# Optimization experiments

Hardware: AMD Instinct MI355X
Metric: run time of the kernel (lower is better)

## Reference

```python
import jax, jax.numpy as jnp
import numpy as np

N, E = 50000, 800000
HID, EDIM, HEADS = 256, 64, 8
C = HID // HEADS  # per-head channels = 32
NEG_SLOPE = 0.2
LN_EPS = 1e-5


def setup_inputs() -> dict:
    key = jax.random.key(0)
    ks = jax.random.split(key, 12)
    s = 1.0 / np.sqrt(HID)
    se = 1.0 / np.sqrt(EDIM)
    return {
        "x": jax.random.normal(ks[0], (N, HID), jnp.float32),
        "edge_index": jax.random.randint(ks[1], (2, E), 0, N, jnp.int32),
        "edge_attr": jax.random.normal(ks[2], (E, EDIM), jnp.float32),
        "W": jax.random.uniform(ks[3], (HID, HEADS * C), jnp.float32, -s, s),
        "W_e": jax.random.uniform(ks[4], (EDIM, HEADS * C), jnp.float32, -se, se),
        "att_src": jax.random.normal(ks[5], (HEADS, C), jnp.float32) * 0.1,
        "att_dst": jax.random.normal(ks[6], (HEADS, C), jnp.float32) * 0.1,
        "att_edge": jax.random.normal(ks[7], (HEADS, C), jnp.float32) * 0.1,
        "bias": jnp.zeros((HEADS * C,), jnp.float32),
        "gamma": jnp.ones((HID,), jnp.float32),
        "beta": jnp.zeros((HID,), jnp.float32),
    }


def _gat_block(x, edge_index, edge_attr, W, W_e, att_src, att_dst, att_edge, bias, gamma, beta):
    n = x.shape[0]
    src, dst = edge_index[0], edge_index[1]
    # node projection (shared for src/dst, as in PyG GATConv non-bipartite)
    xp = (x @ W).reshape(n, HEADS, C)                       # [N,H,C]
    a_src = jnp.einsum("nhc,hc->nh", xp, att_src)          # [N,H]
    a_dst = jnp.einsum("nhc,hc->nh", xp, att_dst)          # [N,H]
    ep = (edge_attr @ W_e).reshape(-1, HEADS, C)            # [E,H,C]
    a_edge = jnp.einsum("ehc,hc->eh", ep, att_edge)        # [E,H]
    # per-edge attention logit + LeakyReLU
    alpha = a_src[src] + a_dst[dst] + a_edge                # [E,H]
    alpha = jax.nn.leaky_relu(alpha, NEG_SLOPE)
    # segment softmax over incoming edges of each dst node
    m = jax.ops.segment_max(alpha, dst, num_segments=n)     # [N,H]
    m = jnp.where(jnp.isfinite(m), m, 0.0)
    ea = jnp.exp(alpha - m[dst])
    den = jax.ops.segment_sum(ea, dst, num_segments=n)      # [N,H]
    attn = ea / (den[dst] + 1e-16)                          # [E,H]
    # weighted message + scatter-add
    msg = xp[src] * attn[:, :, None]                        # [E,H,C]
    out = jax.ops.segment_sum(msg, dst, num_segments=n)     # [N,H,C]
    h = out.reshape(n, HEADS * C) + bias
    # residual + LayerNorm (dropout in eval mode -> identity)
    y = x + h
    mu = jnp.mean(y, axis=-1, keepdims=True)
    var = jnp.var(y, axis=-1, keepdims=True)
    return (y - mu) * jax.lax.rsqrt(var + LN_EPS) * gamma + beta


def reference(x, edge_index, edge_attr, W, W_e, att_src, att_dst, att_edge, bias, gamma, beta):
    return _gat_block(x, edge_index, edge_attr, W, W_e, att_src, att_dst, att_edge, bias, gamma, beta)
```

## Files before the change

kernel.cpp:

```cpp
#include <hip/hip_runtime.h>
#include <cstdint>

#define NEG_SLOPE 0.2f
#define LN_EPS 1e-5f

typedef __bf16 bf16x8 __attribute__((ext_vector_type(8)));
typedef float f32x4 __attribute__((ext_vector_type(4)));

__device__ __forceinline__ float b2f(unsigned int u) {
    union { unsigned int i; float f; } x; x.i = u << 16; return x.f;
}
__device__ __forceinline__ unsigned short f2b(float f) {
    union { float f; unsigned int i; } x; x.f = f;
    unsigned int r = x.i + 0x7fffu + ((x.i >> 16) & 1u);
    return (unsigned short)(r >> 16);
}

__global__ void k0a_prep(const float* __restrict__ W,
                         const float* __restrict__ We,
                         const float* __restrict__ att_src,
                         const float* __restrict__ att_dst,
                         const float* __restrict__ att_edge,
                         float* __restrict__ u_src, float* __restrict__ u_dst,
                         float* __restrict__ vW) {
    int t = threadIdx.x;
    const float* wr = W + t * 256;
    for (int h = 0; h < 8; h++) {
        float s1 = 0.f, s2 = 0.f;
        for (int c = 0; c < 32; c++) {
            float w = wr[h * 32 + c];
            s1 += w * att_src[h * 32 + c];
            s2 += w * att_dst[h * 32 + c];
        }
        u_src[t * 8 + h] = s1; u_dst[t * 8 + h] = s2;
    }
    if (t < 64) {
        const float* er = We + t * 256;
        for (int h = 0; h < 8; h++) {
            float s = 0.f;
            for (int c = 0; c < 32; c++) s += er[h * 32 + c] * att_edge[h * 32 + c];
            vW[t * 8 + h] = s;
        }
    }
}

__global__ void k0b_wfrag(const float* __restrict__ W,
                          unsigned short* __restrict__ Wf) {
    int T = blockIdx.x * 256 + threadIdx.x;
    int j    = T & 7;
    int lane = (T >> 3) & 63;
    int kk   = (T >> 9) & 7;
    int i    = (T >> 12) & 3;
    int w    = T >> 14;
    int n = w * 64 + i * 16 + (lane & 15);
    int k = kk * 32 + (lane >> 4) * 8 + j;
    Wf[T] = f2b(W[k * 256 + n]);
}

__global__ __launch_bounds__(256) void k_deg(const int* __restrict__ ei,
                                             int* __restrict__ deg, int E) {
    int e = blockIdx.x * 256 + threadIdx.x;
    if (e < E) atomicAdd(deg + ei[E + e], 1);
}

__global__ __launch_bounds__(256) void k1_xp(const float* __restrict__ x,
                                             const unsigned short* __restrict__ Wf,
                                             const float* __restrict__ u_src,
                                             const float* __restrict__ u_dst,
                                             unsigned short* __restrict__ xp,
                                             float* __restrict__ a_src,
                                             float* __restrict__ a_dst, int N) {
    __shared__ float red[2][4][16][8];
    int m0 = blockIdx.x * 16;
    int lane = threadIdx.x & 63, wave = threadIdx.x >> 6;
    int quad = lane >> 4, l16 = lane & 15;
    int mrow = m0 + l16; if (mrow > N - 1) mrow = N - 1;
    const float* ap = x + (size_t)mrow * 256 + quad * 8;
    const unsigned short* wfw = Wf + (size_t)wave * 16384;
    f32x4 ac0 = {0,0,0,0}, ac1 = {0,0,0,0}, ac2 = {0,0,0,0}, ac3 = {0,0,0,0};
    float pas[8] = {0,0,0,0,0,0,0,0}, pad_[8] = {0,0,0,0,0,0,0,0};
#pragma unroll
    for (int kk = 0; kk < 8; kk++) {
        float4 fa0 = *(const float4*)(ap + kk * 32);
        float4 fa1 = *(const float4*)(ap + kk * 32 + 4);
        if ((kk >> 1) == wave) {
            float f[8] = {fa0.x, fa0.y, fa0.z, fa0.w, fa1.x, fa1.y, fa1.z, fa1.w};
#pragma unroll
            for (int j = 0; j < 8; j++) {
                int k = kk * 32 + quad * 8 + j;
                const float4* up = (const float4*)(u_src + k * 8);
                float4 s0 = up[0], s1 = up[1];
                const float4* vp = (const float4*)(u_dst + k * 8);
                float4 d0 = vp[0], d1 = vp[1];
                pas[0] += f[j] * s0.x; pas[1] += f[j] * s0.y;
                pas[2] += f[j] * s0.z; pas[3] += f[j] * s0.w;
                pas[4] += f[j] * s1.x; pas[5] += f[j] * s1.y;
                pas[6] += f[j] * s1.z; pas[7] += f[j] * s1.w;
                pad_[0] += f[j] * d0.x; pad_[1] += f[j] * d0.y;
                pad_[2] += f[j] * d0.z; pad_[3] += f[j] * d0.w;
                pad_[4] += f[j] * d1.x; pad_[5] += f[j] * d1.y;
                pad_[6] += f[j] * d1.z; pad_[7] += f[j] * d1.w;
            }
        }
        union { unsigned short u[8]; bf16x8 v; } A;
        A.u[0] = f2b(fa0.x); A.u[1] = f2b(fa0.y); A.u[2] = f2b(fa0.z); A.u[3] = f2b(fa0.w);
        A.u[4] = f2b(fa1.x); A.u[5] = f2b(fa1.y); A.u[6] = f2b(fa1.z); A.u[7] = f2b(fa1.w);
        const unsigned short* wk = wfw + kk * 512 + lane * 8;
        bf16x8 b0 = *(const bf16x8*)(wk);
        bf16x8 b1 = *(const bf16x8*)(wk + 4096);
        bf16x8 b2 = *(const bf16x8*)(wk + 8192);
        bf16x8 b3 = *(const bf16x8*)(wk + 12288);
        ac0 = __builtin_amdgcn_mfma_f32_16x16x32_bf16(A.v, b0, ac0, 0, 0, 0);
        ac1 = __builtin_amdgcn_mfma_f32_16x16x32_bf16(A.v, b1, ac1, 0, 0, 0);
        ac2 = __builtin_amdgcn_mfma_f32_16x16x32_bf16(A.v, b2, ac2, 0, 0, 0);
        ac3 = __builtin_amdgcn_mfma_f32_16x16x32_bf16(A.v, b3, ac3, 0, 0, 0);
    }
#pragma unroll
    for (int h = 0; h < 8; h++) {
        pas[h] += __shfl_xor(pas[h], 16, 64);
        pas[h] += __shfl_xor(pas[h], 32, 64);
        pad_[h] += __shfl_xor(pad_[h], 16, 64);
        pad_[h] += __shfl_xor(pad_[h], 32, 64);
    }
    if (quad == 0) {
#pragma unroll
        for (int h = 0; h < 8; h++) {
            red[0][wave][l16][h] = pas[h];
            red[1][wave][l16][h] = pad_[h];
        }
    }
    int nb = wave * 64;
#pragma unroll
    for (int r = 0; r < 4; r++) {
        int m = m0 + quad * 4 + r;
        if (m < N) {
            unsigned short* op = xp + (size_t)m * 256 + nb + l16;
            op[0]  = f2b(ac0[r]); op[16] = f2b(ac1[r]);
            op[32] = f2b(ac2[r]); op[48] = f2b(ac3[r]);
        }
    }
    __syncthreads();
    {
        int t = threadIdx.x;
        int arr = t >> 7, r = (t >> 3) & 15, h = t & 7;
        int m = m0 + r;
        if (m < N) {
            float sum = red[arr][0][r][h] + red[arr][1][r][h]
                      + red[arr][2][r][h] + red[arr][3][r][h];
            (arr ? a_dst : a_src)[m * 8 + h] = sum;
        }
    }
}

__global__ __launch_bounds__(256) void k2_edge(const int* __restrict__ ei,
                                               const float* __restrict__ eattr,
                                               const float* __restrict__ vW,
                                               const float* __restrict__ a_src,
                                               const float* __restrict__ a_dst,
                                               int* __restrict__ cursor,
                                               int* __restrict__ srcs,
                                               uint4* __restrict__ eav, int E) {
    __shared__ float sv[2048];
    int t = threadIdx.x;
    if (t < 128) {
        const float4* g = (const float4*)vW;
        float4* s4 = (float4*)sv;
        int k = t >> 1, half = t & 1;
        int kl = ((k & 15) << 2) | (k >> 4);
        s4[kl * 2 + half] = g[t];
    }
    __syncthreads();
    int e = blockIdx.x * 64 + (t >> 2), kp = t & 3;
    if (e >= E) return;
    const float4* ar = (const float4*)(eattr + (size_t)e * 64 + kp * 16);
    float acc[8] = {0,0,0,0,0,0,0,0};
#pragma unroll
    for (int q = 0; q < 4; q++) {
        float4 u = ar[q];
        float f[4] = {u.x, u.y, u.z, u.w};
#pragma unroll
        for (int j = 0; j < 4; j++) {
            int kl = ((q * 4 + j) << 2) | kp;
            const float4* vp = (const float4*)(sv + kl * 8);
            float4 v0 = vp[0], v1 = vp[1];
            acc[0] += f[j] * v0.x; acc[1] += f[j] * v0.y;
            acc[2] += f[j] * v0.z; acc[3] += f[j] * v0.w;
            acc[4] += f[j] * v1.x; acc[5] += f[j] * v1.y;
            acc[6] += f[j] * v1.z; acc[7] += f[j] * v1.w;
        }
    }
#pragma unroll
    for (int h = 0; h < 8; h++) {
        acc[h] += __shfl_xor(acc[h], 1, 64);
        acc[h] += __shfl_xor(acc[h], 2, 64);
    }
    int s = ei[e], d = ei[E + e];
    float2 asv = *(const float2*)(a_src + s * 8 + kp * 2);
    float2 adv = *(const float2*)(a_dst + d * 8 + kp * 2);
    float l0 = asv.x + adv.x + acc[kp * 2];
    float l1 = asv.y + adv.y + acc[kp * 2 + 1];
    l0 = (l0 > 0.f) ? l0 : NEG_SLOPE * l0;
    l1 = (l1 > 0.f) ? l1 : NEG_SLOPE * l1;
    unsigned int pk = (unsigned)f2b(__expf(l0)) | ((unsigned)f2b(__expf(l1)) << 16);
    int l = t & 63;
    int p = 0;
    if (kp == 0) p = atomicAdd(cursor + d, 1);
    p = __shfl(p, l & 60, 64);
    ((unsigned int*)eav)[(size_t)p * 4 + kp] = pk;
    if (kp == 0) srcs[p] = s;
}

__global__ __launch_bounds__(1024) void k3a_scan(const int* __restrict__ deg,
                                                 int* __restrict__ rowptr,
                                                 int* __restrict__ bsum, int N) {
    __shared__ int s[1024];
    int t = threadIdx.x, i = blockIdx.x * 1024 + t;
    int v = (i < N) ? deg[i] : 0;
    s[t] = v; __syncthreads();
    for (int off = 1; off < 1024; off <<= 1) {
        int add = (t >= off) ? s[t - off] : 0;
        __syncthreads();
        s[t] += add;
        __syncthreads();
    }
    if (i < N) rowptr[i] = s[t] - v;
    if (t == 1023) bsum[blockIdx.x] = s[1023];
}
__global__ void k3b_scan(const int* __restrict__ bsum, int* __restrict__ boff, int nb) {
    int l = threadIdx.x;
    int v = (l < nb) ? bsum[l] : 0;
    int x = v;
#pragma unroll
    for (int off = 1; off < 64; off <<= 1) {
        int y = __shfl_up(x, off, 64);
        if (l >= off) x += y;
    }
    if (l < nb) boff[l] = x - v;
}
__global__ __launch_bounds__(1024) void k3c_add(int* __restrict__ rowptr,
                                                int* __restrict__ cursor,
                                                const int* __restrict__ boff, int N, int E) {
    int i = blockIdx.x * 1024 + threadIdx.x;
    if (i < N) {
        int r = rowptr[i] + boff[blockIdx.x];
        rowptr[i] = r; cursor[i] = r;
    }
    if (i == 0) rowptr[N] = E;
}

__global__ __launch_bounds__(256) void k4_agg(const float* __restrict__ xin,
                                              const unsigned short* __restrict__ xp,
                                              const int* __restrict__ srcs,
                                              const uint4* __restrict__ eav,
                                              const int* __restrict__ rowptr,
                                              const float* __restrict__ bias,
                                              const float* __restrict__ gamma,
                                              const float* __restrict__ beta,
                                              float* __restrict__ out, int N) {
    __shared__ int ssrc[64];
    __shared__ float sea[64 * 9];
    __shared__ float racc[4][64][4];
    __shared__ float rden[8];
    int n = blockIdx.x;
    int t = threadIdx.x, wave = t >> 6, l = t & 63;
    int start = rowptr[n], end = rowptr[n + 1];
    int hh = l >> 3;
    float a0 = 0.f, a1 = 0.f, a2 = 0.f, a3 = 0.f;
    float den[8] = {0,0,0,0,0,0,0,0};
    for (int base = start; base < end; base += 64) {
        int cnt = end - base; if (cnt > 64) cnt = 64;
        if (t < cnt) {
            ssrc[t] = srcs[base + t];
            uint4 u = eav[base + t];
            float v0 = b2f(u.x & 0xffffu), v1 = b2f(u.x >> 16);
            float v2 = b2f(u.y & 0xffffu), v3 = b2f(u.y >> 16);
            float v4 = b2f(u.z & 0xffffu), v5 = b2f(u.z >> 16);
            float v6 = b2f(u.w & 0xffffu), v7 = b2f(u.w >> 16);
            float* sp = sea + t * 9;
            sp[0] = v0; sp[1] = v1; sp[2] = v2; sp[3] = v3;
            sp[4] = v4; sp[5] = v5; sp[6] = v6; sp[7] = v7;
            den[0] += v0; den[1] += v1; den[2] += v2; den[3] += v3;
            den[4] += v4; den[5] += v5; den[6] += v6; den[7] += v7;
        }
        __syncthreads();
        int i = wave;
        for (; i + 12 < cnt; i += 16) {
            int s0 = ssrc[i], s1 = ssrc[i + 4], s2 = ssrc[i + 8], s3 = ssrc[i + 12];
            uint2 u0 = *(const uint2*)(xp + (size_t)s0 * 256 + l * 4);
            uint2 u1 = *(const uint2*)(xp + (size_t)s1 * 256 + l * 4);
            uint2 u2 = *(const uint2*)(xp + (size_t)s2 * 256 + l * 4);
            uint2 u3 = *(const uint2*)(xp + (size_t)s3 * 256 + l * 4);
            float w0 = sea[i * 9 + hh],        w1 = sea[(i + 4) * 9 + hh];
            float w2 = sea[(i + 8) * 9 + hh],  w3 = sea[(i + 12) * 9 + hh];
            a0 += b2f(u0.x & 0xffffu) * w0; a1 += b2f(u0.x >> 16) * w0;
            a2 += b2f(u0.y & 0xffffu) * w0; a3 += b2f(u0.y >> 16) * w0;
            a0 += b2f(u1.x & 0xffffu) * w1; a1 += b2f(u1.x >> 16) * w1;
            a2 += b2f(u1.y & 0xffffu) * w1; a3 += b2f(u1.y >> 16) * w1;
            a0 += b2f(u2.x & 0xffffu) * w2; a1 += b2f(u2.x >> 16) * w2;
            a2 += b2f(u2.y & 0xffffu) * w2; a3 += b2f(u2.y >> 16) * w2;
            a0 += b2f(u3.x & 0xffffu) * w3; a1 += b2f(u3.x >> 16) * w3;
            a2 += b2f(u3.y & 0xffffu) * w3; a3 += b2f(u3.y >> 16) * w3;
        }
        for (; i + 4 < cnt; i += 8) {
            int s0 = ssrc[i], s1 = ssrc[i + 4];
            uint2 u0 = *(const uint2*)(xp + (size_t)s0 * 256 + l * 4);
            uint2 u1 = *(const uint2*)(xp + (size_t)s1 * 256 + l * 4);
            float w0 = sea[i * 9 + hh], w1 = sea[(i + 4) * 9 + hh];
            a0 += b2f(u0.x & 0xffffu) * w0; a1 += b2f(u0.x >> 16) * w0;
            a2 += b2f(u0.y & 0xffffu) * w0; a3 += b2f(u0.y >> 16) * w0;
            a0 += b2f(u1.x & 0xffffu) * w1; a1 += b2f(u1.x >> 16) * w1;
            a2 += b2f(u1.y & 0xffffu) * w1; a3 += b2f(u1.y >> 16) * w1;
        }
        for (; i < cnt; i += 4) {
            int s0 = ssrc[i];
            uint2 u0 = *(const uint2*)(xp + (size_t)s0 * 256 + l * 4);
            float w0 = sea[i * 9 + hh];
            a0 += b2f(u0.x & 0xffffu) * w0; a1 += b2f(u0.x >> 16) * w0;
            a2 += b2f(u0.y & 0xffffu) * w0; a3 += b2f(u0.y >> 16) * w0;
        }
        __syncthreads();
    }
    racc[wave][l][0] = a0; racc[wave][l][1] = a1;
    racc[wave][l][2] = a2; racc[wave][l][3] = a3;
    if (wave == 0) {
#pragma unroll
        for (int off = 32; off > 0; off >>= 1) {
#pragma unroll
            for (int j = 0; j < 8; j++) den[j] += __shfl_xor(den[j], off, 64);
        }
        if (l < 8) rden[l] = den[l];
    }
    __syncthreads();
    if (wave != 0) return;
    float m0 = racc[0][l][0] + racc[1][l][0] + racc[2][l][0] + racc[3][l][0];
    float m1 = racc[0][l][1] + racc[1][l][1] + racc[2][l][1] + racc[3][l][1];
    float m2 = racc[0][l][2] + racc[1][l][2] + racc[2][l][2] + racc[3][l][2];
    float m3 = racc[0][l][3] + racc[1][l][3] + racc[2][l][3] + racc[3][l][3];
    float sinv = 1.0f / (rden[hh] + 1e-16f);
    m0 *= sinv; m1 *= sinv; m2 *= sinv; m3 *= sinv;
    float4 xv = *(const float4*)(xin + (size_t)n * 256 + l * 4);
    float4 bv = *(const float4*)(bias + l * 4);
    float y0 = xv.x + m0 + bv.x;
    float y1 = xv.y + m1 + bv.y;
    float y2 = xv.z + m2 + bv.z;
    float y3 = xv.w + m3 + bv.w;
    float s1 = y0 + y1 + y2 + y3;
    float s2 = y0 * y0 + y1 * y1 + y2 * y2 + y3 * y3;
#pragma unroll
    for (int o = 32; o > 0; o >>= 1) {
        s1 += __shfl_down(s1, o, 64);
        s2 += __shfl_down(s2, o, 64);
    }
    s1 = __shfl(s1, 0, 64); s2 = __shfl(s2, 0, 64);
    float mu = s1 * (1.f / 256.f);
    float var = s2 * (1.f / 256.f) - mu * mu;
    float rs = rsqrtf(var + LN_EPS);
    float4 gv  = *(const float4*)(gamma + l * 4);
    float4 btv = *(const float4*)(beta + l * 4);
    float4 ov;
    ov.x = (y0 - mu) * rs * gv.x + btv.x;
    ov.y = (y1 - mu) * rs * gv.y + btv.y;
    ov.z = (y2 - mu) * rs * gv.z + btv.z;
    ov.w = (y3 - mu) * rs * gv.w + btv.w;
    *(float4*)(out + (size_t)n * 256 + l * 4) = ov;
}

extern "C" void kernel_launch(void* const* d_in, const int* in_sizes, int n_in,
                              void* d_out, int out_size, void* d_ws, size_t ws_size,
                              hipStream_t stream) {
    const float* x     = (const float*)d_in[0];
    const int*   ei    = (const int*)d_in[1];
    const float* eattr = (const float*)d_in[2];
    const float* W     = (const float*)d_in[3];
    const float* We    = (const float*)d_in[4];
    const float* atts  = (const float*)d_in[5];
    const float* attd  = (const float*)d_in[6];
    const float* atte  = (const float*)d_in[7];
    const float* bias  = (const float*)d_in[8];
    const float* gamma = (const float*)d_in[9];
    const float* beta  = (const float*)d_in[10];
    float* out = (float*)d_out;
    int N = in_sizes[0] / 256;
    int E = in_sizes[1] / 2;

    char* p = (char*)d_ws;
    auto carve = [&](size_t bytes) -> void* {
        void* r = (void*)p; p += (bytes + 255) & ~(size_t)255; return r;
    };
    unsigned short* xp = (unsigned short*)carve((size_t)N * 256 * 2);
    uint4* eav         = (uint4*)carve((size_t)E * 16);
    int*   srcs        = (int*)carve((size_t)E * 4);
    float* a_src       = (float*)carve((size_t)N * 8 * 4);
    float* a_dst       = (float*)carve((size_t)N * 8 * 4);
    int*   deg         = (int*)carve((size_t)N * 4);
    int*   rowptr      = (int*)carve((size_t)(N + 1) * 4);
    int*   cursor      = (int*)carve((size_t)N * 4);
    int*   bsum        = (int*)carve(1024);
    int*   boff        = (int*)carve(1024);
    float* u_src       = (float*)carve(2048 * 4);
    float* u_dst       = (float*)carve(2048 * 4);
    float* vW          = (float*)carve(512 * 4);
    unsigned short* Wf = (unsigned short*)carve(65536 * 2);

    hipMemsetAsync(deg, 0, (size_t)N * 4, stream);

    hipLaunchKernelGGL(k0a_prep, dim3(1), dim3(256), 0, stream,
                       W, We, atts, attd, atte, u_src, u_dst, vW);
    hipLaunchKernelGGL(k0b_wfrag, dim3(256), dim3(256), 0, stream, W, Wf);
    hipLaunchKernelGGL(k_deg, dim3((E + 255) / 256), dim3(256), 0, stream, ei, deg, E);
    int nb = (N + 1023) / 1024;
    hipLaunchKernelGGL(k3a_scan, dim3(nb), dim3(1024), 0, stream, deg, rowptr, bsum, N);
    hipLaunchKernelGGL(k3b_scan, dim3(1), dim3(64), 0, stream, bsum, boff, nb);
    hipLaunchKernelGGL(k3c_add, dim3(nb), dim3(1024), 0, stream, rowptr, cursor, boff, N, E);
    hipLaunchKernelGGL(k1_xp, dim3((N + 15) / 16), dim3(256), 0, stream,
                       x, Wf, u_src, u_dst, xp, a_src, a_dst, N);
    hipLaunchKernelGGL(k2_edge, dim3((E + 63) / 64), dim3(256), 0, stream,
                       ei, eattr, vW, a_src, a_dst, cursor, srcs, eav, E);
    hipLaunchKernelGGL(k4_agg, dim3(N), dim3(256), 0, stream,
                       x, xp, srcs, eav, rowptr, bias, gamma, beta, out, N);
}
```

Before: 610.6 us.

## Merge prep kernels, widen xp GEMM tile, compute attention logits from accumulators

Combines the degree count, weight-fragment packing and edge-attention vector prep into one launch, which removes two kernel launches. The node projection kernel now handles 64 rows per block, so each loaded W fragment is reused across four row groups. It computes a_src and a_dst directly from the bf16-MFMA fp32 accumulators through shuffle reductions instead of a separate fp32 dot with precomputed u vectors. This drops the u_src/u_dst precompute and the shared-memory reduction, but the logits now come from bf16-rounded inputs, a small numerical change. Output stores switch to hardware bf16 conversion.

```diff
diff --git a/kernel.cpp b/kernel.cpp
--- a/kernel.cpp
+++ b/kernel.cpp
@@ -15,139 +15,147 @@
     unsigned int r = x.i + 0x7fffu + ((x.i >> 16) & 1u);
     return (unsigned short)(r >> 16);
 }
-
-__global__ void k0a_prep(const float* __restrict__ W,
-                         const float* __restrict__ We,
-                         const float* __restrict__ att_src,
-                         const float* __restrict__ att_dst,
-                         const float* __restrict__ att_edge,
-                         float* __restrict__ u_src, float* __restrict__ u_dst,
-                         float* __restrict__ vW) {
-    int t = threadIdx.x;
-    const float* wr = W + t * 256;
-    for (int h = 0; h < 8; h++) {
-        float s1 = 0.f, s2 = 0.f;
-        for (int c = 0; c < 32; c++) {
-            float w = wr[h * 32 + c];
-            s1 += w * att_src[h * 32 + c];
-            s2 += w * att_dst[h * 32 + c];
-        }
-        u_src[t * 8 + h] = s1; u_dst[t * 8 + h] = s2;
-    }
-    if (t < 64) {
-        const float* er = We + t * 256;
-        for (int h = 0; h < 8; h++) {
-            float s = 0.f;
-            for (int c = 0; c < 32; c++) s += er[h * 32 + c] * att_edge[h * 32 + c];
-            vW[t * 8 + h] = s;
-        }
-    }
-}
-
-__global__ void k0b_wfrag(const float* __restrict__ W,
-                          unsigned short* __restrict__ Wf) {
-    int T = blockIdx.x * 256 + threadIdx.x;
-    int j    = T & 7;
-    int lane = (T >> 3) & 63;
-    int kk   = (T >> 9) & 7;
-    int i    = (T >> 12) & 3;
-    int w    = T >> 14;
-    int n = w * 64 + i * 16 + (lane & 15);
-    int k = kk * 32 + (lane >> 4) * 8 + j;
-    Wf[T] = f2b(W[k * 256 + n]);
-}
-
-__global__ __launch_bounds__(256) void k_deg(const int* __restrict__ ei,
-                                             int* __restrict__ deg, int E) {
-    int e = blockIdx.x * 256 + threadIdx.x;
-    if (e < E) atomicAdd(deg + ei[E + e], 1);
+__device__ __forceinline__ unsigned short f2b_hw(float f) {
+    __bf16 b = (__bf16)f;
+    union { __bf16 b; unsigned short u; } x; x.b = b; return x.u;
+}
+
+__global__ __launch_bounds__(256) void k0_prep(const int* __restrict__ ei,
+                                               const float* __restrict__ W,
+                                               const float* __restrict__ We,
+                                               const float* __restrict__ att_edge,
+                                               int* __restrict__ deg,
+                                               unsigned short* __restrict__ Wf,
+                                               float* __restrict__ vW,
+                                               int E, int nDegBlocks) {
+    int b = blockIdx.x;
+    if (b < nDegBlocks) {
+        int e = b * 256 + threadIdx.x;
+        if (e < E) atomicAdd(deg + ei[E + e], 1);
+    } else if (b < nDegBlocks + 256) {
+        int T = (b - nDegBlocks) * 256 + threadIdx.x;
+        int j    = T & 7;
+        int lane = (T >> 3) & 63;
+        int kk   = (T >> 9) & 7;
+        int i    = (T >> 12) & 3;
+        int w    = T >> 14;
+        int n = w * 64 + i * 16 + (lane & 15);
+        int k = kk * 32 + (lane >> 4) * 8 + j;
+        Wf[T] = f2b(W[k * 256 + n]);
+    } else {
+        int t = threadIdx.x;
+        if (t < 64) {
+            const float* er = We + t * 256;
+            for (int h = 0; h < 8; h++) {
+                float s = 0.f;
+                for (int c = 0; c < 32; c++) s += er[h * 32 + c] * att_edge[h * 32 + c];
+                vW[t * 8 + h] = s;
+            }
+        }
+    }
 }
 
 __global__ __launch_bounds__(256) void k1_xp(const float* __restrict__ x,
                                              const unsigned short* __restrict__ Wf,
-                                             const float* __restrict__ u_src,
-                                             const float* __restrict__ u_dst,
+                                             const float* __restrict__ att_src,
+                                             const float* __restrict__ att_dst,
                                              unsigned short* __restrict__ xp,
                                              float* __restrict__ a_src,
                                              float* __restrict__ a_dst, int N) {
-    __shared__ float red[2][4][16][8];
-    int m0 = blockIdx.x * 16;
+    int m0 = blockIdx.x * 64;
     int lane = threadIdx.x & 63, wave = threadIdx.x >> 6;
     int quad = lane >> 4, l16 = lane & 15;
-    int mrow = m0 + l16; if (mrow > N - 1) mrow = N - 1;
-    const float* ap = x + (size_t)mrow * 256 + quad * 8;
     const unsigned short* wfw = Wf + (size_t)wave * 16384;
-    f32x4 ac0 = {0,0,0,0}, ac1 = {0,0,0,0}, ac2 = {0,0,0,0}, ac3 = {0,0,0,0};
-    float pas[8] = {0,0,0,0,0,0,0,0}, pad_[8] = {0,0,0,0,0,0,0,0};
+    const float* ap[4];
+#pragma unroll
+    for (int g = 0; g < 4; g++) {
+        int mrow = m0 + g * 16 + l16; if (mrow > N - 1) mrow = N - 1;
+        ap[g] = x + (size_t)mrow * 256 + quad * 8;
+    }
+    f32x4 acc[4][4];
+#pragma unroll
+    for (int g = 0; g < 4; g++)
+#pragma unroll
+        for (int i = 0; i < 4; i++) acc[g][i] = (f32x4){0, 0, 0, 0};
+
 #pragma unroll
     for (int kk = 0; kk < 8; kk++) {
-        float4 fa0 = *(const float4*)(ap + kk * 32);
-        float4 fa1 = *(const float4*)(ap + kk * 32 + 4);
-        if ((kk >> 1) == wave) {
-            float f[8] = {fa0.x, fa0.y, fa0.z, fa0.w, fa1.x, fa1.y, fa1.z, fa1.w};
-#pragma unroll
-            for (int j = 0; j < 8; j++) {
-                int k = kk * 32 + quad * 8 + j;
-                const float4* up = (const float4*)(u_src + k * 8);
-                float4 s0 = up[0], s1 = up[1];
-                const float4* vp = (const float4*)(u_dst + k * 8);
-                float4 d0 = vp[0], d1 = vp[1];
-                pas[0] += f[j] * s0.x; pas[1] += f[j] * s0.y;
-                pas[2] += f[j] * s0.z; pas[3] += f[j] * s0.w;
-                pas[4] += f[j] * s1.x; pas[5] += f[j] * s1.y;
-                pas[6] += f[j] * s1.z; pas[7] += f[j] * s1.w;
-                pad_[0] += f[j] * d0.x; pad_[1] += f[j] * d0.y;
-                pad_[2] += f[j] * d0.z; pad_[3] += f[j] * d0.w;
-                pad_[4] += f[j] * d1.x; pad_[5] += f[j] * d1.y;
-                pad_[6] += f[j] * d1.z; pad_[7] += f[j] * d1.w;
-            }
-        }
-        union { unsigned short u[8]; bf16x8 v; } A;
-        A.u[0] = f2b(fa0.x); A.u[1] = f2b(fa0.y); A.u[2] = f2b(fa0.z); A.u[3] = f2b(fa0.w);
-        A.u[4] = f2b(fa1.x); A.u[5] = f2b(fa1.y); A.u[6] = f2b(fa1.z); A.u[7] = f2b(fa1.w);
         const unsigned short* wk = wfw + kk * 512 + lane * 8;
         bf16x8 b0 = *(const bf16x8*)(wk);
         bf16x8 b1 = *(const bf16x8*)(wk + 4096);
         bf16x8 b2 = *(const bf16x8*)(wk + 8192);
         bf16x8 b3 = *(const bf16x8*)(wk + 12288);
-        ac0 = __builtin_amdgcn_mfma_f32_16x16x32_bf16(A.v, b0, ac0, 0, 0, 0);
-        ac1 = __builtin_amdgcn_mfma_f32_16x16x32_bf16(A.v, b1, ac1, 0, 0, 0);
-        ac2 = __builtin_amdgcn_mfma_f32_16x16x32_bf16(A.v, b2, ac2, 0, 0, 0);
-        ac3 = __builtin_amdgcn_mfma_f32_16x16x32_bf16(A.v, b3, ac3, 0, 0, 0);
-    }
-#pragma unroll
-    for (int h = 0; h < 8; h++) {
-        pas[h] += __shfl_xor(pas[h], 16, 64);
-        pas[h] += __shfl_xor(pas[h], 32, 64);
-        pad_[h] += __shfl_xor(pad_[h], 16, 64);
-        pad_[h] += __shfl_xor(pad_[h], 32, 64);
-    }
-    if (quad == 0) {
-#pragma unroll
-        for (int h = 0; h < 8; h++) {
-            red[0][wave][l16][h] = pas[h];
-            red[1][wave][l16][h] = pad_[h];
-        }
-    }
+#pragma unroll
+        for (int g = 0; g < 4; g++) {
+            float4 fa0 = *(const float4*)(ap[g] + kk * 32);
+            float4 fa1 = *(const float4*)(ap[g] + kk * 32 + 4);
+            bf16x8 Av;
+            Av[0] = (__bf16)fa0.x; Av[1] = (__bf16)fa0.y;
+            Av[2] = (__bf16)fa0.z; Av[3] = (__bf16)fa0.w;
+            Av[4] = (__bf16)fa1.x; Av[5] = (__bf16)fa1.y;
+            Av[6] = (__bf16)fa1.z; Av[7] = (__bf16)fa1.w;
+            acc[g][0] = __builtin_amdgcn_mfma_f32_16x16x32_bf16(Av, b0, acc[g][0], 0, 0, 0);
+            acc[g][1] = __builtin_amdgcn_mfma_f32_16x16x32_bf16(Av, b1, acc[g][1], 0, 0, 0);
+            acc[g][2] = __builtin_amdgcn_mfma_f32_16x16x32_bf16(Av, b2, acc[g][2], 0, 0, 0);
+            acc[g][3] = __builtin_amdgcn_mfma_f32_16x16x32_bf16(Av, b3, acc[g][3], 0, 0, 0);
+        }
+    }
+
     int nb = wave * 64;
 #pragma unroll
-    for (int r = 0; r < 4; r++) {
-        int m = m0 + quad * 4 + r;
-        if (m < N) {
-            unsigned short* op = xp + (size_t)m * 256 + nb + l16;
-            op[0]  = f2b(ac0[r]); op[16] = f2b(ac1[r]);
-            op[32] = f2b(ac2[r]); op[48] = f2b(ac3[r]);
-        }
-    }
-    __syncthreads();
-    {
-        int t = threadIdx.x;
-        int arr = t >> 7, r = (t >> 3) & 15, h = t & 7;
-        int m = m0 + r;
-        if (m < N) {
-            float sum = red[arr][0][r][h] + red[arr][1][r][h]
-                      + red[arr][2][r][h] + red[arr][3][r][h];
-            (arr ? a_dst : a_src)[m * 8 + h] = sum;
+    for (int g = 0; g < 4; g++) {
+#pragma unroll
+        for (int r = 0; r < 4; r++) {
+            int m = m0 + g * 16 + quad * 4 + r;
+            if (m < N) {
+                unsigned short* op = xp + (size_t)m * 256 + nb + l16;
+                op[0]  = f2b_hw(acc[g][0][r]); op[16] = f2b_hw(acc[g][1][r]);
+                op[32] = f2b_hw(acc[g][2][r]); op[48] = f2b_hw(acc[g][3][r]);
+            }
+        }
+    }
+
+    float asv[4], adv[4];
+#pragma unroll
+    for (int i = 0; i < 4; i++) {
+        int h = wave * 2 + (i >> 1);
+        int c = (i & 1) * 16 + l16;
+        asv[i] = att_src[h * 32 + c];
+        adv[i] = att_dst[h * 32 + c];
+    }
+#pragma unroll
+    for (int g = 0; g < 4; g++) {
+#pragma unroll
+        for (int hb = 0; hb < 2; hb++) {
+            f32x4 ps = {0, 0, 0, 0}, pd = {0, 0, 0, 0};
+#pragma unroll
+            for (int ii = 0; ii < 2; ii++) {
+                int i = hb * 2 + ii;
+#pragma unroll
+                for (int r = 0; r < 4; r++) {
+                    ps[r] += acc[g][i][r] * asv[i];
+                    pd[r] += acc[g][i][r] * adv[i];
+                }
+            }
+#pragma unroll
+            for (int off = 1; off < 16; off <<= 1) {
+#pragma unroll
+                for (int r = 0; r < 4; r++) {
+                    ps[r] += __shfl_xor(ps[r], off, 64);
+                    pd[r] += __shfl_xor(pd[r], off, 64);
+                }
+            }
+            if (l16 == 0) {
+                int h = wave * 2 + hb;
+#pragma unroll
+                for (int r = 0; r < 4; r++) {
+                    int m = m0 + g * 16 + quad * 4 + r;
+                    if (m < N) {
+                        a_src[(size_t)m * 8 + h] = ps[r];
+                        a_dst[(size_t)m * 8 + h] = pd[r];
+                    }
+                }
+            }
         }
     }
 }
@@ -397,23 +405,20 @@
     int*   cursor      = (int*)carve((size_t)N * 4);
     int*   bsum        = (int*)carve(1024);
     int*   boff        = (int*)carve(1024);
-    float* u_src       = (float*)carve(2048 * 4);
-    float* u_dst       = (float*)carve(2048 * 4);
     float* vW          = (float*)carve(512 * 4);
     unsigned short* Wf = (unsigned short*)carve(65536 * 2);
 
     hipMemsetAsync(deg, 0, (size_t)N * 4, stream);
 
-    hipLaunchKernelGGL(k0a_prep, dim3(1), dim3(256), 0, stream,
-                       W, We, atts, attd, atte, u_src, u_dst, vW);
-    hipLaunchKernelGGL(k0b_wfrag, dim3(256), dim3(256), 0, stream, W, Wf);
-    hipLaunchKernelGGL(k_deg, dim3((E + 255) / 256), dim3(256), 0, stream, ei, deg, E);
+    int nDeg = (E + 255) / 256;
+    hipLaunchKernelGGL(k0_prep, dim3(nDeg + 257), dim3(256), 0, stream,
+                       ei, W, We, atte, deg, Wf, vW, E, nDeg);
     int nb = (N + 1023) / 1024;
     hipLaunchKernelGGL(k3a_scan, dim3(nb), dim3(1024), 0, stream, deg, rowptr, bsum, N);
     hipLaunchKernelGGL(k3b_scan, dim3(1), dim3(64), 0, stream, bsum, boff, nb);
     hipLaunchKernelGGL(k3c_add, dim3(nb), dim3(1024), 0, stream, rowptr, cursor, boff, N, E);
-    hipLaunchKernelGGL(k1_xp, dim3((N + 15) / 16), dim3(256), 0, stream,
-                       x, Wf, u_src, u_dst, xp, a_src, a_dst, N);
+    hipLaunchKernelGGL(k1_xp, dim3((N + 63) / 64), dim3(256), 0, stream,
+                       x, Wf, atts, attd, xp, a_src, a_dst, N);
     hipLaunchKernelGGL(k2_edge, dim3((E + 63) / 64), dim3(256), 0, stream,
                        ei, eattr, vW, a_src, a_dst, cursor, srcs, eav, E);
     hipLaunchKernelGGL(k4_agg, dim3(N), dim3(256), 0, stream,
```

Measured after the change: 545.6 us. -10.6%, faster.
